# Kernel tuning notes

Measured on AMD Instinct MI355X. Metric: run time of the kernel, lower is better.

The kernel has to match this reference:

```python
import jax, jax.numpy as jnp
import numpy as np

N, IN_DIM, OUT_DIM, HEADS = 8192, 256, 128, 2


def setup_inputs() -> dict:
    key = jax.random.key(0)
    k1, k2, k3, k4, k5 = jax.random.split(key, 5)
    features = jax.random.normal(k1, (N, IN_DIM), dtype=jnp.float32)
    adjacency = jax.random.randint(k2, (N, N), 0, 2, dtype=jnp.int32)
    # nn.Linear(input_dim, output_dim*heads, bias=False): weight [out, in]
    W = jax.random.normal(k3, (OUT_DIM * HEADS, IN_DIM), dtype=jnp.float32) * 0.05
    attn_src = jax.random.normal(k4, (HEADS, OUT_DIM), dtype=jnp.float32) * 0.05
    attn_dst = jax.random.normal(k5, (HEADS, OUT_DIM), dtype=jnp.float32) * 0.05
    return {"features": features, "adjacency": adjacency, "W": W,
            "attn_src": attn_src, "attn_dst": attn_dst}


def reference(features, adjacency, W, attn_src, attn_dst):
    n = features.shape[0]
    # transformed: [N, H, F]
    transformed = (features @ W.T).reshape(n, HEADS, OUT_DIM)
    src_scores = jnp.einsum('nhf,hf->nh', transformed, attn_src)  # [N, H]
    dst_scores = jnp.einsum('nhf,hf->nh', transformed, attn_dst)  # [N, H]
    # logits: [N_src, N_dst, H]
    logits = jax.nn.leaky_relu(src_scores[:, None, :] + dst_scores[None, :, :],
                               negative_slope=0.2)
    mask = adjacency > 0  # [N, N]
    logits = jnp.where(mask[:, :, None], logits, -jnp.inf)
    attention = jax.nn.softmax(logits, axis=1)  # softmax over dst dim (dim=1)
    attention = jnp.nan_to_num(attention, nan=0.0, posinf=0.0, neginf=0.0)
    aggregated = jnp.einsum('ijh,jhf->ihf', attention, transformed)  # [N, H, F]
    return aggregated.mean(axis=1)  # [N, F]
```

## Files before the change

kernel.cpp:

```cpp
#include <hip/hip_runtime.h>
#include <stdint.h>
#include <stddef.h>

#define NN 8192
#define KD 256
#define CD 256
#define FD 128
#define BI 64
#define BJ 64

typedef __attribute__((ext_vector_type(4))) float f32x4;
typedef __attribute__((ext_vector_type(8))) short b16x8;

__device__ __forceinline__ unsigned short f2bf(float x) {
    unsigned int u = __float_as_uint(x);
    u += 0x7fffu + ((u >> 16) & 1u);
    return (unsigned short)(u >> 16);
}

__device__ __forceinline__ void async16(const void* g, void* l) {
    __builtin_amdgcn_global_load_lds(
        (const __attribute__((address_space(1))) unsigned int*)g,
        (__attribute__((address_space(3))) unsigned int*)l, 16, 0, 0);
}

__global__ __launch_bounds__(256) void k_transform(
    const float* __restrict__ feat, const float* __restrict__ W,
    const float* __restrict__ asrc, const float* __restrict__ adst,
    unsigned short* __restrict__ Tt, float* __restrict__ s, float* __restrict__ d)
{
    __shared__ unsigned short a_lds[64 * 32];
    __shared__ unsigned short b_lds[256 * 32];
    __shared__ unsigned short tr_lds[256 * 72];
    __shared__ float sc_lds[4][64];
    __shared__ float dc_lds[4][64];

    const int t = threadIdx.x;
    const int wave = t >> 6, lane = t & 63;
    const int l15 = lane & 15, quad = lane >> 4;
    const int n0 = blockIdx.x * 64;
    const int ai = t >> 2, ag = t & 3;

    f32x4 acc[4][4] = {};
    for (int kc = 0; kc < 8; ++kc) {
        const int k0 = kc * 32;
        __syncthreads();
        {
            const float* src = feat + (size_t)(n0 + ai) * KD + k0 + ag * 8;
            const float4 v0 = *(const float4*)src;
            const float4 v1 = *(const float4*)(src + 4);
            union { unsigned short us[8]; b16x8 v; } pk;
            pk.us[0] = f2bf(v0.x); pk.us[1] = f2bf(v0.y);
            pk.us[2] = f2bf(v0.z); pk.us[3] = f2bf(v0.w);
            pk.us[4] = f2bf(v1.x); pk.us[5] = f2bf(v1.y);
            pk.us[6] = f2bf(v1.z); pk.us[7] = f2bf(v1.w);
            const int slot = ag ^ ((ai >> 1) & 3);
            *(b16x8*)&a_lds[ai * 32 + slot * 8] = pk.v;
        }
        for (int p = 0; p < 4; ++p) {
            const int G = p * 256 + t;
            const int c = G >> 2, g = G & 3;
            const float* src = W + (size_t)c * KD + k0 + g * 8;
            const float4 v0 = *(const float4*)src;
            const float4 v1 = *(const float4*)(src + 4);
            union { unsigned short us[8]; b16x8 v; } pk;
            pk.us[0] = f2bf(v0.x); pk.us[1] = f2bf(v0.y);
            pk.us[2] = f2bf(v0.z); pk.us[3] = f2bf(v0.w);
            pk.us[4] = f2bf(v1.x); pk.us[5] = f2bf(v1.y);
            pk.us[6] = f2bf(v1.z); pk.us[7] = f2bf(v1.w);
            const int slot = g ^ ((c >> 1) & 3);
            *(b16x8*)&b_lds[c * 32 + slot * 8] = pk.v;
        }
        __syncthreads();
        b16x8 af[4], bfr[4];
        for (int mt = 0; mt < 4; ++mt) {
            const int m = mt * 16 + l15;
            af[mt] = *(const b16x8*)&a_lds[m * 32 + (quad ^ ((m >> 1) & 3)) * 8];
        }
        for (int nt = 0; nt < 4; ++nt) {
            const int c = wave * 64 + nt * 16 + l15;
            bfr[nt] = *(const b16x8*)&b_lds[c * 32 + (quad ^ ((c >> 1) & 3)) * 8];
        }
        for (int mt = 0; mt < 4; ++mt)
            for (int nt = 0; nt < 4; ++nt)
                acc[mt][nt] = __builtin_amdgcn_mfma_f32_16x16x32_bf16(
                    af[mt], bfr[nt], acc[mt][nt], 0, 0, 0);
    }

    float aS[4], aD[4];
    for (int nt = 0; nt < 4; ++nt) {
        const int c = wave * 64 + nt * 16 + l15;
        aS[nt] = asrc[c]; aD[nt] = adst[c];
    }
    for (int mt = 0; mt < 4; ++mt)
        for (int r = 0; r < 4; ++r) {
            float vs = 0.f, vd = 0.f;
            for (int nt = 0; nt < 4; ++nt) {
                const float x = acc[mt][nt][r];
                vs += x * aS[nt]; vd += x * aD[nt];
            }
            vs += __shfl_xor(vs, 1); vd += __shfl_xor(vd, 1);
            vs += __shfl_xor(vs, 2); vd += __shfl_xor(vd, 2);
            vs += __shfl_xor(vs, 4); vd += __shfl_xor(vd, 4);
            vs += __shfl_xor(vs, 8); vd += __shfl_xor(vd, 8);
            if (l15 == 0) {
                const int nl = mt * 16 + quad * 4 + r;
                sc_lds[wave][nl] = vs; dc_lds[wave][nl] = vd;
            }
        }
    for (int mt = 0; mt < 4; ++mt)
        for (int nt = 0; nt < 4; ++nt)
            for (int r = 0; r < 4; ++r) {
                const int c = wave * 64 + nt * 16 + l15;
                const int n = mt * 16 + quad * 4 + r;
                tr_lds[c * 72 + n] = f2bf(acc[mt][nt][r]);
            }
    __syncthreads();
    if (t < 128) {
        const int n = t >> 1, h = t & 1;
        s[(size_t)(n0 + n) * 2 + h] = sc_lds[h * 2][n] + sc_lds[h * 2 + 1][n];
        d[(size_t)(n0 + n) * 2 + h] = dc_lds[h * 2][n] + dc_lds[h * 2 + 1][n];
    }
    for (int p = 0; p < 8; ++p) {
        const int idx = p * 256 + t;
        const int c = idx >> 3, g = idx & 7;
        *(b16x8*)(Tt + (size_t)c * NN + n0 + g * 8) = *(const b16x8*)&tr_lds[c * 72 + g * 8];
    }
}

__global__ __launch_bounds__(512, 4) void k_gat(
    const int* __restrict__ adj, const unsigned short* __restrict__ Tt,
    const float* __restrict__ s, const float* __restrict__ d,
    float* __restrict__ num_part,
    float* __restrict__ den_part,
    int jchunk)
{
    __shared__ unsigned short tt_lds[CD * BJ];
    __shared__ unsigned short w_lds[2 * BI * BJ];

    const int t = threadIdx.x;
    const int w = t >> 6, lane = t & 63;
    const int l15 = lane & 15, quad = lane >> 4;
    const int h  = (w >> 2) & 1;
    const int fh = (w >> 1) & 1;
    const int rh = w & 1;
    const int i0 = blockIdx.x * BI;
    const int chunk = blockIdx.y;
    const int jbase = chunk * jchunk;

    const int wi = t >> 3;
    const int j8 = t & 7;
    const int gi = i0 + wi;
    const float s0 = s[(size_t)gi * 2 + 0];
    const float s1 = s[(size_t)gi * 2 + 1];
    const int cbase = h * 128 + fh * 64;

    f32x4 acc[2][4] = {};
    float den0 = 0.f, den1 = 0.f;
    const int njt = jchunk / BJ;

    const int* arow = adj + (size_t)gi * NN + j8 * 8;
    int4 a0p = *(const int4*)(arow + jbase);
    int4 a1p = *(const int4*)(arow + jbase + 4);

    for (int jt = 0; jt < njt; ++jt) {
        const int j0 = jbase + jt * BJ;
        __syncthreads();
        const float4* dvp = (const float4*)(d + (size_t)(j0 + j8 * 8) * 2);
        union { float4 v[4]; float f[16]; } dv;
        dv.v[0] = dvp[0]; dv.v[1] = dvp[1]; dv.v[2] = dvp[2]; dv.v[3] = dvp[3];
        for (int p = 0; p < 4; ++p) {
            const int G = (p * 8 + w) * 64 + lane;
            const int c = G >> 3, gt = G & 7;
            const int g = gt ^ (c & 7);
            async16(Tt + (size_t)c * NN + j0 + g * 8,
                    (char*)tt_lds + (size_t)(p * 8 + w) * 1024);
        }
        const int jn = (jt + 1 < njt) ? j0 + BJ : jbase;
        const int4 aN0 = *(const int4*)(arow + jn);
        const int4 aN1 = *(const int4*)(arow + jn + 4);
        const int am[8] = {a0p.x, a0p.y, a0p.z, a0p.w, a1p.x, a1p.y, a1p.z, a1p.w};
        union { unsigned short us[8]; b16x8 v; } w0, w1;
        float dp0 = 0.f, dp1 = 0.f;
        for (int e = 0; e < 8; ++e) {
            float x0 = s0 + dv.f[e * 2 + 0];  x0 = x0 > 0.f ? x0 : 0.2f * x0;
            float x1 = s1 + dv.f[e * 2 + 1];  x1 = x1 > 0.f ? x1 : 0.2f * x1;
            const float e0 = am[e] != 0 ? __expf(x0) : 0.f;
            const float e1 = am[e] != 0 ? __expf(x1) : 0.f;
            dp0 += e0; dp1 += e1;
            w0.us[e] = f2bf(e0); w1.us[e] = f2bf(e1);
        }
        den0 += dp0; den1 += dp1;
        const int slot = (j8 ^ (wi & 7)) << 3;
        *(b16x8*)&w_lds[(0 * BI + wi) * BJ + slot] = w0.v;
        *(b16x8*)&w_lds[(1 * BI + wi) * BJ + slot] = w1.v;
        a0p = aN0; a1p = aN1;
        __syncthreads();
        for (int ks = 0; ks < 2; ++ks) {
            const int gidx = ks * 4 + quad;
            b16x8 af[2], bfr[4];
            for (int mt = 0; mt < 2; ++mt) {
                const int m = rh * 32 + mt * 16 + l15;
                af[mt] = *(const b16x8*)&w_lds[(h * BI + m) * BJ + ((gidx ^ (m & 7)) << 3)];
            }
            for (int nt = 0; nt < 4; ++nt) {
                const int c = cbase + nt * 16 + l15;
                bfr[nt] = *(const b16x8*)&tt_lds[c * BJ + ((gidx ^ (c & 7)) << 3)];
            }
            for (int mt = 0; mt < 2; ++mt)
                for (int nt = 0; nt < 4; ++nt)
                    acc[mt][nt] = __builtin_amdgcn_mfma_f32_16x16x32_bf16(
                        af[mt], bfr[nt], acc[mt][nt], 0, 0, 0);
        }
    }
    den0 += __shfl_xor(den0, 1); den0 += __shfl_xor(den0, 2); den0 += __shfl_xor(den0, 4);
    den1 += __shfl_xor(den1, 1); den1 += __shfl_xor(den1, 2); den1 += __shfl_xor(den1, 4);
    if (j8 == 0) {
        den_part[((size_t)chunk * 2 + 0) * NN + gi] = den0;
        den_part[((size_t)chunk * 2 + 1) * NN + gi] = den1;
    }
    float* np_ = num_part + (size_t)chunk * NN * CD;
    for (int mt = 0; mt < 2; ++mt)
        for (int nt = 0; nt < 4; ++nt)
            for (int r = 0; r < 4; ++r) {
                const int n = i0 + rh * 32 + mt * 16 + quad * 4 + r;
                const int c = cbase + nt * 16 + l15;
                np_[(size_t)n * CD + c] = acc[mt][nt][r];
            }
}

__global__ __launch_bounds__(256) void k_combine(
    const float* __restrict__ num_part, const float* __restrict__ den_part,
    float* __restrict__ out, int jsplit)
{
    const int idx = blockIdx.x * 256 + threadIdx.x;
    const int n = idx >> 7, f = idx & 127;
    const size_t row = (size_t)n * CD;
    float n0 = 0.f, n1 = 0.f, d0 = 0.f, d1 = 0.f;
    for (int c = 0; c < jsplit; ++c) {
        const size_t base = (size_t)c * NN * CD;
        n0 += num_part[base + row + f];
        n1 += num_part[base + row + 128 + f];
        d0 += den_part[((size_t)c * 2 + 0) * NN + n];
        d1 += den_part[((size_t)c * 2 + 1) * NN + n];
    }
    const float r0 = d0 != 0.f ? n0 / d0 : 0.f;
    const float r1 = d1 != 0.f ? n1 / d1 : 0.f;
    out[idx] = 0.5f * (r0 + r1);
}

extern "C" void kernel_launch(void* const* d_in, const int* in_sizes, int n_in,
                              void* d_out, int out_size, void* d_ws, size_t ws_size,
                              hipStream_t stream) {
    const float* feat = (const float*)d_in[0];
    const int*   adj  = (const int*)d_in[1];
    const float* W    = (const float*)d_in[2];
    const float* asrc = (const float*)d_in[3];
    const float* adst = (const float*)d_in[4];
    float* out = (float*)d_out;

    const int jsplit = (ws_size >= ((size_t)73 << 20)) ? 8
                     : (ws_size >= ((size_t)40 << 20)) ? 4 : 2;
    const int jchunk = NN / jsplit;

    char* ws = (char*)d_ws;
    unsigned short* Tt = (unsigned short*)ws;
    float* s    = (float*)(ws + ((size_t)4 << 20));
    float* dsc  = (float*)(ws + ((size_t)4 << 20) + (64 << 10));
    float* den  = (float*)(ws + ((size_t)4 << 20) + (128 << 10));
    float* nump = (float*)(ws + ((size_t)8 << 20));

    k_transform<<<128, 256, 0, stream>>>(feat, W, asrc, adst, Tt, s, dsc);
    k_gat<<<dim3(NN / BI, jsplit), 512, 0, stream>>>(adj, Tt, s, dsc, nump, den, jchunk);
    k_combine<<<NN * FD / 256, 256, 0, stream>>>(nump, den, out, jsplit);
}
```

Before: 477.6 us.

## Double-buffer Tt tiles in LDS and prefetch adjacency and scores one tile ahead

Splits the transformed-feature LDS tile into two buffers and issues async loads for the next tile, along with next adjacency and dst-score loads, before computing the current tile. Replaces __syncthreads with raw barriers and an explicit vmcnt wait so prefetches stay in flight during MFMA work. Also caps the j-split at 4 chunks, reducing partial-sum traffic but also block count. The doubled LDS footprint lowers the number of resident blocks per CU.

```diff
diff --git a/kernel.cpp b/kernel.cpp
--- a/kernel.cpp
+++ b/kernel.cpp
@@ -135,7 +135,7 @@
     float* __restrict__ den_part,
     int jchunk)
 {
-    __shared__ unsigned short tt_lds[CD * BJ];
+    __shared__ unsigned short tt_lds[2][CD * BJ];
     __shared__ unsigned short w_lds[2 * BI * BJ];
 
     const int t = threadIdx.x;
@@ -160,26 +160,38 @@
     const int njt = jchunk / BJ;
 
     const int* arow = adj + (size_t)gi * NN + j8 * 8;
-    int4 a0p = *(const int4*)(arow + jbase);
-    int4 a1p = *(const int4*)(arow + jbase + 4);
+
+    for (int p = 0; p < 4; ++p) {
+        const int G = (p * 8 + w) * 64 + lane;
+        const int c = G >> 3, gt = G & 7;
+        const int g = gt ^ (c & 7);
+        async16(Tt + (size_t)c * NN + jbase + g * 8,
+                (char*)&tt_lds[0][0] + (size_t)(p * 8 + w) * 1024);
+    }
+    int4 aC0 = *(const int4*)(arow + jbase);
+    int4 aC1 = *(const int4*)(arow + jbase + 4);
+    const float4* dcp = (const float4*)(d + (size_t)(jbase + j8 * 8) * 2);
+    float4 dC0 = dcp[0], dC1 = dcp[1], dC2 = dcp[2], dC3 = dcp[3];
 
     for (int jt = 0; jt < njt; ++jt) {
         const int j0 = jbase + jt * BJ;
-        __syncthreads();
-        const float4* dvp = (const float4*)(d + (size_t)(j0 + j8 * 8) * 2);
-        union { float4 v[4]; float f[16]; } dv;
-        dv.v[0] = dvp[0]; dv.v[1] = dvp[1]; dv.v[2] = dvp[2]; dv.v[3] = dvp[3];
+        const int cur = jt & 1;
+        __builtin_amdgcn_s_barrier();
+        const int jn = (jt + 1 < njt) ? j0 + BJ : j0;
         for (int p = 0; p < 4; ++p) {
             const int G = (p * 8 + w) * 64 + lane;
             const int c = G >> 3, gt = G & 7;
             const int g = gt ^ (c & 7);
-            async16(Tt + (size_t)c * NN + j0 + g * 8,
-                    (char*)tt_lds + (size_t)(p * 8 + w) * 1024);
-        }
-        const int jn = (jt + 1 < njt) ? j0 + BJ : jbase;
+            async16(Tt + (size_t)c * NN + jn + g * 8,
+                    (char*)&tt_lds[cur ^ 1][0] + (size_t)(p * 8 + w) * 1024);
+        }
         const int4 aN0 = *(const int4*)(arow + jn);
         const int4 aN1 = *(const int4*)(arow + jn + 4);
-        const int am[8] = {a0p.x, a0p.y, a0p.z, a0p.w, a1p.x, a1p.y, a1p.z, a1p.w};
+        const float4* dnp = (const float4*)(d + (size_t)(jn + j8 * 8) * 2);
+        const float4 dN0 = dnp[0], dN1 = dnp[1], dN2 = dnp[2], dN3 = dnp[3];
+        const int am[8] = {aC0.x, aC0.y, aC0.z, aC0.w, aC1.x, aC1.y, aC1.z, aC1.w};
+        union { float4 v[4]; float f[16]; } dv;
+        dv.v[0] = dC0; dv.v[1] = dC1; dv.v[2] = dC2; dv.v[3] = dC3;
         union { unsigned short us[8]; b16x8 v; } w0, w1;
         float dp0 = 0.f, dp1 = 0.f;
         for (int e = 0; e < 8; ++e) {
@@ -194,8 +206,10 @@
         const int slot = (j8 ^ (wi & 7)) << 3;
         *(b16x8*)&w_lds[(0 * BI + wi) * BJ + slot] = w0.v;
         *(b16x8*)&w_lds[(1 * BI + wi) * BJ + slot] = w1.v;
-        a0p = aN0; a1p = aN1;
-        __syncthreads();
+        aC0 = aN0; aC1 = aN1; dC0 = dN0; dC1 = dN1; dC2 = dN2; dC3 = dN3;
+        asm volatile("s_waitcnt vmcnt(10) lgkmcnt(0)" ::: "memory");
+        __builtin_amdgcn_s_barrier();
+        __builtin_amdgcn_sched_barrier(0);
         for (int ks = 0; ks < 2; ++ks) {
             const int gidx = ks * 4 + quad;
             b16x8 af[2], bfr[4];
@@ -205,7 +219,7 @@
             }
             for (int nt = 0; nt < 4; ++nt) {
                 const int c = cbase + nt * 16 + l15;
-                bfr[nt] = *(const b16x8*)&tt_lds[c * BJ + ((gidx ^ (c & 7)) << 3)];
+                bfr[nt] = *(const b16x8*)&tt_lds[cur][c * BJ + ((gidx ^ (c & 7)) << 3)];
             }
             for (int mt = 0; mt < 2; ++mt)
                 for (int nt = 0; nt < 4; ++nt)
@@ -213,6 +227,7 @@
                         af[mt], bfr[nt], acc[mt][nt], 0, 0, 0);
         }
     }
+    asm volatile("s_waitcnt vmcnt(0)" ::: "memory");
     den0 += __shfl_xor(den0, 1); den0 += __shfl_xor(den0, 2); den0 += __shfl_xor(den0, 4);
     den1 += __shfl_xor(den1, 1); den1 += __shfl_xor(den1, 2); den1 += __shfl_xor(den1, 4);
     if (j8 == 0) {
@@ -259,8 +274,7 @@
     const float* adst = (const float*)d_in[4];
     float* out = (float*)d_out;
 
-    const int jsplit = (ws_size >= ((size_t)73 << 20)) ? 8
-                     : (ws_size >= ((size_t)40 << 20)) ? 4 : 2;
+    const int jsplit = (ws_size >= ((size_t)40 << 20)) ? 4 : 2;
     const int jchunk = NN / jsplit;
 
     char* ws = (char*)d_ws;
```

New measurement: 448.7 us. 6.0% less time.
